# Performance work log

Measured on AMD Instinct MI355X. Metric: run time of the kernel, lower is better.

The kernel has to match this reference:

```python
import jax, jax.numpy as jnp
import numpy as np

B, S, H, D = 1, 2048, 24, 128   # batch, img seq, heads, head_dim
RD = 64                          # rotary_emb_dim (partial RoPE)
IPS, IPD = 512, 1152             # ip tokens, ip feature dim
HID = H * D                      # 3072
EPS = 1e-6


def _heads(x):
    # (B, S, H*D) -> (B, H, S, D)
    b, s, _ = x.shape
    return x.reshape(b, s, H, D).transpose(0, 2, 1, 3)


def _rmsnorm(x, scale):
    # RMSNorm with p<0 path: rms = ||x||_2 / sqrt(D); y = scale * x / (rms + eps)
    rms = jnp.linalg.norm(x, axis=-1, keepdims=True) * (D ** -0.5)
    return scale * (x / (rms + EPS))


def _rope(x, sin, cos):
    # rotate-half RoPE on first RD channels, pass-through on the rest
    xr, xp = x[..., :RD], x[..., RD:]
    x1, x2 = jnp.split(xr, 2, axis=-1)
    rot = jnp.concatenate([-x2, x1], axis=-1)
    return jnp.concatenate([xr * cos + rot * sin, xp], axis=-1)


def setup_inputs() -> dict:
    key = jax.random.key(0)
    ks = jax.random.split(key, 16)
    std = 0.02
    inp = {
        "hidden_states": jax.random.normal(ks[0], (B, S, HID), jnp.float32),
        "ip_hidden_states": jax.random.normal(ks[1], (B, IPS, IPD), jnp.float32),
        "sin": jax.random.normal(ks[2], (S, RD), jnp.float32),
        "cos": jax.random.normal(ks[3], (S, RD), jnp.float32),
        "Wq": jax.random.normal(ks[4], (HID, HID), jnp.float32) * std,
        "bq": jnp.zeros((HID,), jnp.float32),
        "Wk": jax.random.normal(ks[5], (HID, HID), jnp.float32) * std,
        "bk": jnp.zeros((HID,), jnp.float32),
        "Wv": jax.random.normal(ks[6], (HID, HID), jnp.float32) * std,
        "bv": jnp.zeros((HID,), jnp.float32),
        "Wo": jax.random.normal(ks[7], (HID, HID), jnp.float32) * std,
        "bo": jnp.zeros((HID,), jnp.float32),
        "Wk_ip": jax.random.normal(ks[8], (HID, IPD), jnp.float32) * std,
        "bk_ip": jnp.zeros((HID,), jnp.float32),
        "Wv_ip": jax.random.normal(ks[9], (HID, IPD), jnp.float32) * std,
        "bv_ip": jnp.zeros((HID,), jnp.float32),
        "q_scale": jnp.ones((D,), jnp.float32),
        "k_scale": jnp.ones((D,), jnp.float32),
    }
    return inp


def reference(hidden_states, ip_hidden_states, sin, cos,
              Wq, bq, Wk, bk, Wv, bv, Wo, bo,
              Wk_ip, bk_ip, Wv_ip, bv_ip, q_scale, k_scale):
    scale = 1.0  # default `scale` kwarg
    # projections (self-attention: encoder_hidden_states = hidden_states)
    q = _heads(hidden_states @ Wq.T + bq)        # (B,H,S,D)
    k = _heads(hidden_states @ Wk.T + bk)
    v = _heads(hidden_states @ Wv.T + bv)
    k_ip = _heads(ip_hidden_states @ Wk_ip.T + bk_ip)   # (B,H,IPS,D)
    v_ip = _heads(ip_hidden_states @ Wv_ip.T + bv_ip)

    # IP branch uses RMS-normed, head_dim^-0.5-scaled, UNROTATED q and k_ip
    # (key_ip is rotated in the source but the rotated value is never used)
    q_norm = _rmsnorm(q, q_scale) * (D ** -0.5)
    k_ip_norm = _rmsnorm(k_ip, k_scale) * (D ** -0.5)

    # main branch: RoPE'd q/k, raw dot product (alpha=1.0, no 1/sqrt(d))
    q_rot = _rope(q, sin, cos)
    k_rot = _rope(k, sin, cos)

    scores = jnp.einsum('bhsd,bhtd->bhst', q_rot, k_rot)
    probs = jax.nn.softmax(scores, axis=-1)
    scores_ip = scale * jnp.einsum('bhsd,bhtd->bhst', q_norm, k_ip_norm)
    probs_ip = jax.nn.softmax(scores_ip, axis=-1)

    out = jnp.einsum('bhst,bhtd->bhsd', probs, v) \
        + jnp.einsum('bhst,bhtd->bhsd', probs_ip, v_ip)
    out = out.transpose(0, 2, 1, 3).reshape(B, S, HID)  # batch_to_head_dim
    out = out @ Wo.T + bo                                # to_out[0]; dropout = id
    return out
```

## Files before the change

### kernel.cpp

```cpp
#include <hip/hip_runtime.h>
#include <stdint.h>

#define S_LEN 2048
#define NH    24
#define HD    128
#define HID   3072
#define IPS   512
#define IPD   1152

using f16   = __fp16;
using f16x4 = __fp16 __attribute__((ext_vector_type(4)));
using f16x8 = __fp16 __attribute__((ext_vector_type(8)));
using f32x4 = float  __attribute__((ext_vector_type(4)));
using f32x16 = float __attribute__((ext_vector_type(16)));

__device__ __forceinline__ void glds16(const f16* g, f16* l) {
  __builtin_amdgcn_global_load_lds((const __attribute__((address_space(1))) void*)g,
                                   (__attribute__((address_space(3))) void*)l,
                                   16, 0, 0);
}

struct CastArgs { const float* src[8]; f16* dst[8]; long n4[8]; };

__global__ void k_cvt_all(CastArgs a, long total4) {
  long i = blockIdx.x * 256L + threadIdx.x;
  if (i >= total4) return;
  long r = i; int s = 0;
  while (r >= a.n4[s]) { r -= a.n4[s]; s++; }
  float4 v = ((const float4*)a.src[s])[r];
  f16x4 o;
  o.x = (f16)v.x; o.y = (f16)v.y; o.z = (f16)v.z; o.w = (f16)v.w;
  ((f16x4*)a.dst[s])[r] = o;
}

struct ProjArgs {
  const f16 *A0, *A1;
  const f16 *Wq, *Wk, *Wv, *Wkip, *Wvip;
  const float *bq, *bk, *bv, *bkip, *bvip;
  f16 *q, *k, *v, *kip, *vip;
};

__global__ __launch_bounds__(256) void k_gemm_proj(ProjArgs pa) {
  const int z = blockIdx.z;
  const f16* A; const f16* B; const float* bias; f16* C; int K;
  if (z == 0)      { A = pa.A0; B = pa.Wq;   bias = pa.bq;   C = pa.q;   K = 3072; }
  else if (z == 1) { A = pa.A0; B = pa.Wk;   bias = pa.bk;   C = pa.k;   K = 3072; }
  else if (z == 2) { A = pa.A0; B = pa.Wv;   bias = pa.bv;   C = pa.v;   K = 3072; }
  else if (z == 3) { if (blockIdx.y >= 4) return;
                     A = pa.A1; B = pa.Wkip; bias = pa.bkip; C = pa.kip; K = 1152; }
  else             { if (blockIdx.y >= 4) return;
                     A = pa.A1; B = pa.Wvip; bias = pa.bvip; C = pa.vip; K = 1152; }

  __shared__ f16 As[128 * 64];
  __shared__ f16 Bs[128 * 64];

  const int tid = threadIdx.x;
  const int w   = tid >> 6, l = tid & 63;
  const int l31 = l & 31, hi = l >> 5;
  const int bm = blockIdx.y * 128, bn = blockIdx.x * 128;
  const int wm = (w >> 1) * 64,    wn = (w & 1) * 64;

  f32x16 acc[2][2] = {};

  const int r0   = w * 32;
  const int srow = l >> 3;
  const int gch  = (l & 7) ^ (srow & 7);
  const f16* Ag = A + (long)(bm + r0 + srow) * K + gch * 8;
  const f16* Bg = B + (long)(bn + r0 + srow) * K + gch * 8;
  f16* lA = &As[r0 * 64];
  f16* lB = &Bs[r0 * 64];
  const long rs8 = 8L * K;
  const int swz = l & 7;

  for (int k0 = 0; k0 < K; k0 += 64) {
#pragma unroll
    for (int g = 0; g < 4; g++) {
      glds16(Ag + g * rs8 + k0, lA + g * 512);
      glds16(Bg + g * rs8 + k0, lB + g * 512);
    }
    __syncthreads();

#pragma unroll
    for (int ks = 0; ks < 4; ks++) {
      const int pos = ((ks * 2 + hi) ^ swz) * 8;
      f16x8 af[2], bf[2];
#pragma unroll
      for (int mi = 0; mi < 2; mi++)
        af[mi] = *(const f16x8*)&As[(wm + mi * 32 + l31) * 64 + pos];
#pragma unroll
      for (int nj = 0; nj < 2; nj++)
        bf[nj] = *(const f16x8*)&Bs[(wn + nj * 32 + l31) * 64 + pos];
#pragma unroll
      for (int mi = 0; mi < 2; mi++)
#pragma unroll
        for (int nj = 0; nj < 2; nj++)
          acc[mi][nj] = __builtin_amdgcn_mfma_f32_32x32x16_f16(af[mi], bf[nj], acc[mi][nj], 0, 0, 0);
    }
    __syncthreads();
  }

#pragma unroll
  for (int mi = 0; mi < 2; mi++)
#pragma unroll
    for (int nj = 0; nj < 2; nj++) {
      const int col = bn + wn + nj * 32 + l31;
      const float bvv = bias[col];
      const int rowb = bm + wm + mi * 32 + 4 * hi;
#pragma unroll
      for (int reg = 0; reg < 16; reg++) {
        const int row = rowb + (reg & 3) + 8 * (reg >> 2);
        C[(long)row * HID + col] = (f16)(acc[mi][nj][reg] + bvv);
      }
    }
}

__global__ __launch_bounds__(256) void k_gemm_nt(
    const f16* __restrict__ A, const f16* __restrict__ B,
    const float* __restrict__ bias, float* __restrict__ Cv,
    int M, int N, int K)
{
  __shared__ f16 As[128 * 64];
  __shared__ f16 Bs[128 * 64];

  const int tid = threadIdx.x;
  const int w   = tid >> 6, l = tid & 63;
  const int l31 = l & 31, hi = l >> 5;
  const int bm = blockIdx.y * 128, bn = blockIdx.x * 128;
  const int wm = (w >> 1) * 64,    wn = (w & 1) * 64;

  f32x16 acc[2][2] = {};

  const int r0   = w * 32;
  const int srow = l >> 3;
  const int gch  = (l & 7) ^ (srow & 7);
  const f16* Ag = A + (long)(bm + r0 + srow) * K + gch * 8;
  const f16* Bg = B + (long)(bn + r0 + srow) * K + gch * 8;
  f16* lA = &As[r0 * 64];
  f16* lB = &Bs[r0 * 64];
  const long rs8 = 8L * K;
  const int swz = l & 7;

  for (int k0 = 0; k0 < K; k0 += 64) {
#pragma unroll
    for (int g = 0; g < 4; g++) {
      glds16(Ag + g * rs8 + k0, lA + g * 512);
      glds16(Bg + g * rs8 + k0, lB + g * 512);
    }
    __syncthreads();

#pragma unroll
    for (int ks = 0; ks < 4; ks++) {
      const int pos = ((ks * 2 + hi) ^ swz) * 8;
      f16x8 af[2], bf[2];
#pragma unroll
      for (int mi = 0; mi < 2; mi++)
        af[mi] = *(const f16x8*)&As[(wm + mi * 32 + l31) * 64 + pos];
#pragma unroll
      for (int nj = 0; nj < 2; nj++)
        bf[nj] = *(const f16x8*)&Bs[(wn + nj * 32 + l31) * 64 + pos];
#pragma unroll
      for (int mi = 0; mi < 2; mi++)
#pragma unroll
        for (int nj = 0; nj < 2; nj++)
          acc[mi][nj] = __builtin_amdgcn_mfma_f32_32x32x16_f16(af[mi], bf[nj], acc[mi][nj], 0, 0, 0);
    }
    __syncthreads();
  }

#pragma unroll
  for (int mi = 0; mi < 2; mi++)
#pragma unroll
    for (int nj = 0; nj < 2; nj++) {
      const int col = bn + wn + nj * 32 + l31;
      const float bvv = bias[col];
      const int rowb = bm + wm + mi * 32 + 4 * hi;
#pragma unroll
      for (int reg = 0; reg < 16; reg++) {
        const int row = rowb + (reg & 3) + 8 * (reg >> 2);
        Cv[(long)row * N + col] = acc[mi][nj][reg] + bvv;
      }
    }
}

__global__ void k_qprep(const f16* __restrict__ x, const float* __restrict__ snp,
                        const float* __restrict__ csp, const float* __restrict__ scale,
                        f16* __restrict__ qrot, f16* __restrict__ qnorm, int rows) {
  int gw = (blockIdx.x * 256 + threadIdx.x) >> 6;
  int l  = threadIdx.x & 63;
  if (gw >= rows) return;
  long base = (long)gw * HD;
  int s = gw / NH;
  int d = 2 * l;
  float a = (float)x[base + d];
  float b = (float)x[base + d + 1];

  float ss = a * a + b * b;
#pragma unroll
  for (int off = 32; off >= 1; off >>= 1) ss += __shfl_xor(ss, off, 64);
  float rms = sqrtf(ss * (1.0f / HD));
  float inv = 0.08838834764831845f / (rms + 1e-6f);
  qnorm[base + d]     = (f16)(a * scale[d] * inv);
  qnorm[base + d + 1] = (f16)(b * scale[d + 1] * inv);

  float pa = __shfl_xor(a, 16, 64);
  float pb = __shfl_xor(b, 16, 64);
  float ra, rb;
  if (d < 64) {
    float sgn = (d < 32) ? -1.0f : 1.0f;
    ra = a * csp[s * 64 + d]     + sgn * pa * snp[s * 64 + d];
    rb = b * csp[s * 64 + d + 1] + sgn * pb * snp[s * 64 + d + 1];
  } else {
    ra = a; rb = b;
  }
  qrot[base + d]     = (f16)ra;
  qrot[base + d + 1] = (f16)rb;
}

__global__ void k_krope_pack(const f16* __restrict__ src, const float* __restrict__ snp,
                             const float* __restrict__ csp, f16* __restrict__ dst,
                             int T, int nchunk) {
  int i = blockIdx.x * 256 + threadIdx.x;
  if (i >= nchunk) return;
  int d8 = i % 384;
  int t  = i / 384;
  int h  = d8 >> 4;
  int d  = (d8 & 15) * 8;
  f16x8 x = *(const f16x8*)(src + (long)i * 8);
  f16x8 o;
  if (d < 64) {
    f16x8 p = (d < 32) ? *(const f16x8*)(src + (long)i * 8 + 32)
                       : *(const f16x8*)(src + (long)i * 8 - 32);
    float sgn = (d < 32) ? -1.0f : 1.0f;
#pragma unroll
    for (int j = 0; j < 8; j++) {
      float cs = csp[t * 64 + d + j], sn = snp[t * 64 + d + j];
      o[j] = (f16)((float)x[j] * cs + sgn * (float)p[j] * sn);
    }
  } else {
    o = x;
  }
  long off = ((((long)h * (T >> 4) + (t >> 4)) * 4 + (d >> 5)) * 64 + ((d >> 3) & 3) * 16 + (t & 15)) * 8;
  *(f16x8*)(dst + off) = o;
}

__global__ void k_rms_pack(const f16* __restrict__ x, const float* __restrict__ scale,
                           f16* __restrict__ dst, int T, int rows) {
  int gw  = (blockIdx.x * 256 + threadIdx.x) >> 6;
  int l   = threadIdx.x & 63;
  int sub = l >> 4, l16 = l & 15;
  int row = gw * 4 + sub;
  if (row >= rows) return;
  int t = row / NH, h = row - t * NH;
  int d = l16 * 8;
  f16x8 v = *(const f16x8*)(x + (long)row * HD + d);
  float ss = 0.f;
#pragma unroll
  for (int j = 0; j < 8; j++) { float f = (float)v[j]; ss += f * f; }
  ss += __shfl_xor(ss, 1, 64);
  ss += __shfl_xor(ss, 2, 64);
  ss += __shfl_xor(ss, 4, 64);
  ss += __shfl_xor(ss, 8, 64);
  float rms = sqrtf(ss * (1.0f / HD));
  float inv = 0.08838834764831845f / (rms + 1e-6f);
  f16x8 o;
#pragma unroll
  for (int j = 0; j < 8; j++) o[j] = (f16)((float)v[j] * scale[d + j] * inv);
  long off = ((((long)h * (T >> 4) + (t >> 4)) * 4 + (d >> 5)) * 64 + ((d >> 3) & 3) * 16 + (t & 15)) * 8;
  *(f16x8*)(dst + off) = o;
}

__global__ __launch_bounds__(256) void k_vpack(const f16* __restrict__ v, f16* __restrict__ dst, int T) {
  __shared__ f16 Ts[128 * 72];
  int h = blockIdx.y, tb = blockIdx.x, t0 = tb * 64;
  int tid = threadIdx.x;
  int r = tid >> 2, c4 = tid & 3;
#pragma unroll
  for (int cc = 0; cc < 4; cc++) {
    int ch = c4 * 4 + cc;
    f16x8 x = *(const f16x8*)(v + (long)(t0 + r) * HID + h * HD + ch * 8);
#pragma unroll
    for (int j = 0; j < 8; j++)
      Ts[(ch * 8 + j) * 72 + r] = x[j];
  }
  __syncthreads();
  int l16 = tid & 15, jd = (tid >> 4) & 7, ks = tid >> 7;
#pragma unroll
  for (int quad = 0; quad < 4; quad++) {
    f16x8 x = *(const f16x8*)&Ts[(jd * 16 + l16) * 72 + ks * 32 + quad * 8];
    long off = ((((long)h * (T >> 6) + tb) * 2 + ks) * 8 + jd) * 512 + (quad * 16 + l16) * 8;
    *(f16x8*)(dst + off) = x;
  }
}

__global__ __launch_bounds__(256, 3) void k_flash2(
    const f16* __restrict__ Q, const f16* __restrict__ Kp, const f16* __restrict__ Vp,
    f16* __restrict__ Opart, long part_stride, float2* __restrict__ ml, int p0,
    int T, int Tc)
{
  __shared__ f16 Ps[4][32 * 72];

  const int h    = blockIdx.y;
  const int sp   = blockIdx.z;
  const int tid  = threadIdx.x, w = tid >> 6, l = tid & 63;
  const int quad = l >> 4, l16 = l & 15;
  const int qr   = blockIdx.x * 128 + w * 32;
  const int Tt16 = T >> 4, Tt64 = T >> 6;

  f16x8 qf[2][4];
#pragma unroll
  for (int mt = 0; mt < 2; mt++)
#pragma unroll
    for (int kq = 0; kq < 4; kq++)
      qf[mt][kq] = *(const f16x8*)(Q + (long)(qr + mt * 16 + l16) * HID + h * HD + kq * 32 + quad * 8);

  f32x4 o[2][8] = {};
  float m_run[8], l_run[8];
#pragma unroll
  for (int i = 0; i < 8; i++) { m_run[i] = -1e30f; l_run[i] = 0.f; }

  f16* myP = &Ps[w][0];
  const int t_begin = sp * Tc, t_end = t_begin + Tc;

  for (int t0 = t_begin; t0 < t_end; t0 += 64) {
    f32x4 s[2][4] = {};
#pragma unroll
    for (int kq = 0; kq < 4; kq++) {
      f16x8 kf[4];
#pragma unroll
      for (int jn = 0; jn < 4; jn++)
        kf[jn] = *(const f16x8*)(Kp + (((long)(h * Tt16 + (t0 >> 4) + jn) * 4 + kq) * 64 + l) * 8);
#pragma unroll
      for (int mt = 0; mt < 2; mt++)
#pragma unroll
        for (int jn = 0; jn < 4; jn++)
          s[mt][jn] = __builtin_amdgcn_mfma_f32_16x16x32_f16(qf[mt][kq], kf[jn], s[mt][jn], 0, 0, 0);
    }

#pragma unroll
    for (int mt = 0; mt < 2; mt++) {
#pragma unroll
      for (int r = 0; r < 4; r++) {
        float mx = fmaxf(fmaxf(s[mt][0][r], s[mt][1][r]), fmaxf(s[mt][2][r], s[mt][3][r]));
        mx = fmaxf(mx, __shfl_xor(mx, 1, 64));
        mx = fmaxf(mx, __shfl_xor(mx, 2, 64));
        mx = fmaxf(mx, __shfl_xor(mx, 4, 64));
        mx = fmaxf(mx, __shfl_xor(mx, 8, 64));
        const int ri = mt * 4 + r;
        float mn = fmaxf(m_run[ri], mx);
        float al = __expf(m_run[ri] - mn);
        m_run[ri] = mn;
        float p0v = __expf(s[mt][0][r] - mn);
        float p1v = __expf(s[mt][1][r] - mn);
        float p2v = __expf(s[mt][2][r] - mn);
        float p3v = __expf(s[mt][3][r] - mn);
        s[mt][0][r] = p0v; s[mt][1][r] = p1v; s[mt][2][r] = p2v; s[mt][3][r] = p3v;
        l_run[ri] = l_run[ri] * al + (p0v + p1v + p2v + p3v);
#pragma unroll
        for (int jd = 0; jd < 8; jd++) o[mt][jd][r] *= al;
      }
    }

#pragma unroll
    for (int mt = 0; mt < 2; mt++)
#pragma unroll
      for (int jn = 0; jn < 4; jn++)
#pragma unroll
        for (int r = 0; r < 4; r++)
          myP[(mt * 16 + quad * 4 + r) * 72 + jn * 16 + l16] = (f16)s[mt][jn][r];

#pragma unroll
    for (int ks = 0; ks < 2; ks++) {
      f16x8 pf[2];
#pragma unroll
      for (int mt = 0; mt < 2; mt++)
        pf[mt] = *(const f16x8*)&myP[(mt * 16 + l16) * 72 + ks * 32 + quad * 8];
      f16x8 vf[8];
#pragma unroll
      for (int jd = 0; jd < 8; jd++)
        vf[jd] = *(const f16x8*)(Vp + ((((long)(h * Tt64 + (t0 >> 6)) * 2 + ks) * 8 + jd) * 64 + l) * 8);
#pragma unroll
      for (int jd = 0; jd < 8; jd++)
#pragma unroll
        for (int mt = 0; mt < 2; mt++)
          o[mt][jd] = __builtin_amdgcn_mfma_f32_16x16x32_f16(pf[mt], vf[jd], o[mt][jd], 0, 0, 0);
    }
  }

#pragma unroll
  for (int i = 0; i < 8; i++) {
    float v = l_run[i];
    v += __shfl_xor(v, 1, 64);
    v += __shfl_xor(v, 2, 64);
    v += __shfl_xor(v, 4, 64);
    v += __shfl_xor(v, 8, 64);
    l_run[i] = v;
  }

  f16* Od = Opart + (long)sp * part_stride;
#pragma unroll
  for (int mt = 0; mt < 2; mt++)
#pragma unroll
    for (int jd = 0; jd < 8; jd++)
#pragma unroll
      for (int r = 0; r < 4; r++) {
        int row = qr + mt * 16 + quad * 4 + r;
        int col = h * HD + jd * 16 + l16;
        Od[(long)row * HID + col] = (f16)o[mt][jd][r];
      }
  if (l16 == 0) {
#pragma unroll
    for (int mt = 0; mt < 2; mt++)
#pragma unroll
      for (int r = 0; r < 4; r++) {
        int row = qr + mt * 16 + quad * 4 + r;
        float2 v; v.x = m_run[mt * 4 + r]; v.y = l_run[mt * 4 + r];
        ml[((long)(p0 + sp) * NH + h) * S_LEN + row] = v;
      }
  }
}

__global__ void k_combine(const f16* __restrict__ O0, const f16* __restrict__ O1,
                          const f16* __restrict__ O2, const f16* __restrict__ O3,
                          const f16* __restrict__ O4, const f16* __restrict__ O5,
                          const float2* __restrict__ ml, f16* __restrict__ out, int nchunk) {
  int i = blockIdx.x * 256 + threadIdx.x;
  if (i >= nchunk) return;
  int s = i / 384, d8 = i - s * 384, h = d8 >> 4;
  long base = (long)h * S_LEN + s;
  float2 a0 = ml[0 * NH * S_LEN + base];
  float2 a1 = ml[1L * NH * S_LEN + base];
  float2 a2 = ml[2L * NH * S_LEN + base];
  float2 a3 = ml[3L * NH * S_LEN + base];
  float2 a4 = ml[4L * NH * S_LEN + base];
  float2 a5 = ml[5L * NH * S_LEN + base];
  float M1 = fmaxf(fmaxf(a0.x, a1.x), fmaxf(a2.x, a3.x));
  float e0 = __expf(a0.x - M1), e1 = __expf(a1.x - M1), e2 = __expf(a2.x - M1), e3 = __expf(a3.x - M1);
  float L1 = a0.y * e0 + a1.y * e1 + a2.y * e2 + a3.y * e3;
  float w0 = e0 / L1, w1 = e1 / L1, w2 = e2 / L1, w3 = e3 / L1;
  float M2 = fmaxf(a4.x, a5.x);
  float e4 = __expf(a4.x - M2), e5 = __expf(a5.x - M2);
  float L2 = a4.y * e4 + a5.y * e5;
  float w4 = e4 / L2, w5 = e5 / L2;
  f16x8 v0 = ((const f16x8*)O0)[i];
  f16x8 v1 = ((const f16x8*)O1)[i];
  f16x8 v2 = ((const f16x8*)O2)[i];
  f16x8 v3 = ((const f16x8*)O3)[i];
  f16x8 v4 = ((const f16x8*)O4)[i];
  f16x8 v5 = ((const f16x8*)O5)[i];
  f16x8 r;
#pragma unroll
  for (int j = 0; j < 8; j++) {
    float acc = w0 * (float)v0[j] + w1 * (float)v1[j] + w2 * (float)v2[j] + w3 * (float)v3[j]
              + w4 * (float)v4[j] + w5 * (float)v5[j];
    r[j] = (f16)acc;
  }
  ((f16x8*)out)[i] = r;
}

extern "C" void kernel_launch(void* const* d_in, const int* in_sizes, int n_in,
                              void* d_out, int out_size, void* d_ws, size_t ws_size,
                              hipStream_t stream) {
  const float* hs   = (const float*)d_in[0];
  const float* ip   = (const float*)d_in[1];
  const float* snp  = (const float*)d_in[2];
  const float* csp  = (const float*)d_in[3];
  const float* Wq   = (const float*)d_in[4];
  const float* bq   = (const float*)d_in[5];
  const float* Wk   = (const float*)d_in[6];
  const float* bk   = (const float*)d_in[7];
  const float* Wv   = (const float*)d_in[8];
  const float* bv   = (const float*)d_in[9];
  const float* Wo   = (const float*)d_in[10];
  const float* bo   = (const float*)d_in[11];
  const float* Wkip = (const float*)d_in[12];
  const float* bkip = (const float*)d_in[13];
  const float* Wvip = (const float*)d_in[14];
  const float* bvip = (const float*)d_in[15];
  const float* qs   = (const float*)d_in[16];
  const float* ks   = (const float*)d_in[17];
  float* out = (float*)d_out;

  const long n1   = 6291456;
  const long nW   = 9437184;
  const long nip  = 589824;
  const long nWip = 3538944;

  const long o_hs   = 0;
  const long o_Wq   = 6291456;
  const long o_Wk   = 15728640;
  const long o_Wv   = 25165824;
  const long o_Wo   = 34603008;
  const long o_ip   = 44040192;
  const long o_Wkip = 44630016;
  const long o_Wvip = 48168960;
  const long o_q    = 51707904;
  const long o_k    = 57999360;
  const long o_v    = 64290816;
  const long o_kip  = 70582272;
  const long o_vip  = 72155136;
  const long o_qrot = 73728000;
  const long o_qnorm= 80019456;
  const long o_Vpip = 87883776;
  const long o_ml   = 89456640;
  const long o_Kps  = o_hs;
  const long o_Op0  = o_Wq;
  const long o_Op4  = o_Wkip;
  const long o_Op5  = o_q;
  const long o_Vps  = o_k;
  const long o_Kpip = o_kip;
  const long o_attn = o_v;

  f16* WS = (f16*)d_ws;
  auto P = [&](long off) { return WS + off; };
  float2* mlp = (float2*)(WS + o_ml);

  CastArgs ca;
  ca.src[0] = hs;   ca.dst[0] = P(o_hs);   ca.n4[0] = n1 / 4;
  ca.src[1] = ip;   ca.dst[1] = P(o_ip);   ca.n4[1] = nip / 4;
  ca.src[2] = Wq;   ca.dst[2] = P(o_Wq);   ca.n4[2] = nW / 4;
  ca.src[3] = Wk;   ca.dst[3] = P(o_Wk);   ca.n4[3] = nW / 4;
  ca.src[4] = Wv;   ca.dst[4] = P(o_Wv);   ca.n4[4] = nW / 4;
  ca.src[5] = Wo;   ca.dst[5] = P(o_Wo);   ca.n4[5] = nW / 4;
  ca.src[6] = Wkip; ca.dst[6] = P(o_Wkip); ca.n4[6] = nWip / 4;
  ca.src[7] = Wvip; ca.dst[7] = P(o_Wvip); ca.n4[7] = nWip / 4;
  const long total4 = (n1 + nip + 4 * nW + 2 * nWip) / 4;
  k_cvt_all<<<dim3((total4 + 255) / 256), 256, 0, stream>>>(ca, total4);

  ProjArgs pa;
  pa.A0 = P(o_hs); pa.A1 = P(o_ip);
  pa.Wq = P(o_Wq); pa.Wk = P(o_Wk); pa.Wv = P(o_Wv);
  pa.Wkip = P(o_Wkip); pa.Wvip = P(o_Wvip);
  pa.bq = bq; pa.bk = bk; pa.bv = bv; pa.bkip = bkip; pa.bvip = bvip;
  pa.q = P(o_q); pa.k = P(o_k); pa.v = P(o_v);
  pa.kip = P(o_kip); pa.vip = P(o_vip);
  k_gemm_proj<<<dim3(24, 16, 5), 256, 0, stream>>>(pa);

  k_qprep<<<dim3(49152 / 4), 256, 0, stream>>>(P(o_q), snp, csp, qs, P(o_qrot), P(o_qnorm), 49152);
  k_krope_pack<<<dim3(786432 / 256), 256, 0, stream>>>(P(o_k), snp, csp, P(o_Kps), 2048, 786432);
  k_rms_pack<<<dim3(12288 / 16), 256, 0, stream>>>(P(o_kip), ks, P(o_Kpip), 512, 12288);
  k_vpack<<<dim3(32, 24), 256, 0, stream>>>(P(o_v),   P(o_Vps),  2048);
  k_vpack<<<dim3(8, 24),  256, 0, stream>>>(P(o_vip), P(o_Vpip), 512);

  k_flash2<<<dim3(16, 24, 4), 256, 0, stream>>>(P(o_qrot), P(o_Kps), P(o_Vps),
      P(o_Op0), n1, mlp, 0, 2048, 512);
  k_flash2<<<dim3(16, 24, 2), 256, 0, stream>>>(P(o_qnorm), P(o_Kpip), P(o_Vpip),
      P(o_Op4), o_Op5 - o_Op4, mlp, 4, 512, 256);

  k_combine<<<dim3(786432 / 256), 256, 0, stream>>>(
      P(o_Op0), P(o_Op0 + n1), P(o_Op0 + 2 * n1), P(o_Op0 + 3 * n1),
      P(o_Op4), P(o_Op5), mlp, P(o_attn), 786432);

  k_gemm_nt<<<dim3(24, 16, 1), 256, 0, stream>>>(P(o_attn),
      P(o_Wo), bo, out, 2048, 3072, 3072);
}
```

Measured before the change: 668.4 us.

## Fuse fp32-to-fp16 weight conversion into GEMM B-tile loads; use DPP reductions

The separate cast kernel stops converting the weight matrices to fp16. The projection and output GEMMs now read fp32 weights directly, convert them in registers and store them to LDS, while the activations still use async global-to-LDS loads. This removes a large weight write and re-read pass through memory. In exchange, each GEMM tile reads twice the bytes for B, and the B-tile loads become synchronous register loads with conversion inside the main loop. The flash-attention row max and sum reductions also switch from shuffles to DPP moves.

```diff
diff --git a/kernel.cpp b/kernel.cpp
--- a/kernel.cpp
+++ b/kernel.cpp
@@ -20,29 +20,44 @@
                                    16, 0, 0);
 }
 
-struct CastArgs { const float* src[8]; f16* dst[8]; long n4[8]; };
-
-__global__ void k_cvt_all(CastArgs a, long total4) {
+__device__ __forceinline__ float red16_max(float x) {
+  x = fmaxf(x, __int_as_float(__builtin_amdgcn_mov_dpp(__float_as_int(x), 0xB1, 0xf, 0xf, true)));
+  x = fmaxf(x, __int_as_float(__builtin_amdgcn_mov_dpp(__float_as_int(x), 0x4E, 0xf, 0xf, true)));
+  x = fmaxf(x, __int_as_float(__builtin_amdgcn_mov_dpp(__float_as_int(x), 0x141, 0xf, 0xf, true)));
+  x = fmaxf(x, __int_as_float(__builtin_amdgcn_mov_dpp(__float_as_int(x), 0x140, 0xf, 0xf, true)));
+  return x;
+}
+__device__ __forceinline__ float red16_sum(float x) {
+  x += __int_as_float(__builtin_amdgcn_mov_dpp(__float_as_int(x), 0xB1, 0xf, 0xf, true));
+  x += __int_as_float(__builtin_amdgcn_mov_dpp(__float_as_int(x), 0x4E, 0xf, 0xf, true));
+  x += __int_as_float(__builtin_amdgcn_mov_dpp(__float_as_int(x), 0x141, 0xf, 0xf, true));
+  x += __int_as_float(__builtin_amdgcn_mov_dpp(__float_as_int(x), 0x140, 0xf, 0xf, true));
+  return x;
+}
+
+__global__ void k_cvt2(const float* __restrict__ a, f16* __restrict__ da, long n4a,
+                       const float* __restrict__ b, f16* __restrict__ db, long total4) {
   long i = blockIdx.x * 256L + threadIdx.x;
   if (i >= total4) return;
-  long r = i; int s = 0;
-  while (r >= a.n4[s]) { r -= a.n4[s]; s++; }
-  float4 v = ((const float4*)a.src[s])[r];
+  const float* s; f16* d; long r;
+  if (i < n4a) { s = a; d = da; r = i; }
+  else         { s = b; d = db; r = i - n4a; }
+  float4 v = ((const float4*)s)[r];
   f16x4 o;
   o.x = (f16)v.x; o.y = (f16)v.y; o.z = (f16)v.z; o.w = (f16)v.w;
-  ((f16x4*)a.dst[s])[r] = o;
+  ((f16x4*)d)[r] = o;
 }
 
 struct ProjArgs {
   const f16 *A0, *A1;
-  const f16 *Wq, *Wk, *Wv, *Wkip, *Wvip;
+  const float *Wq, *Wk, *Wv, *Wkip, *Wvip;
   const float *bq, *bk, *bv, *bkip, *bvip;
   f16 *q, *k, *v, *kip, *vip;
 };
 
 __global__ __launch_bounds__(256) void k_gemm_proj(ProjArgs pa) {
   const int z = blockIdx.z;
-  const f16* A; const f16* B; const float* bias; f16* C; int K;
+  const f16* A; const float* B; const float* bias; f16* C; int K;
   if (z == 0)      { A = pa.A0; B = pa.Wq;   bias = pa.bq;   C = pa.q;   K = 3072; }
   else if (z == 1) { A = pa.A0; B = pa.Wk;   bias = pa.bk;   C = pa.k;   K = 3072; }
   else if (z == 2) { A = pa.A0; B = pa.Wv;   bias = pa.bv;   C = pa.v;   K = 3072; }
@@ -65,8 +80,8 @@
   const int r0   = w * 32;
   const int srow = l >> 3;
   const int gch  = (l & 7) ^ (srow & 7);
-  const f16* Ag = A + (long)(bm + r0 + srow) * K + gch * 8;
-  const f16* Bg = B + (long)(bn + r0 + srow) * K + gch * 8;
+  const f16*   Ag = A + (long)(bm + r0 + srow) * K + gch * 8;
+  const float* Bg = B + (long)(bn + r0 + srow) * K + gch * 8;
   f16* lA = &As[r0 * 64];
   f16* lB = &Bs[r0 * 64];
   const long rs8 = 8L * K;
@@ -74,9 +89,17 @@
 
   for (int k0 = 0; k0 < K; k0 += 64) {
 #pragma unroll
+    for (int g = 0; g < 4; g++)
+      glds16(Ag + g * rs8 + k0, lA + g * 512);
+#pragma unroll
     for (int g = 0; g < 4; g++) {
-      glds16(Ag + g * rs8 + k0, lA + g * 512);
-      glds16(Bg + g * rs8 + k0, lB + g * 512);
+      const float* src = Bg + g * rs8 + k0;
+      float4 u0 = *(const float4*)src;
+      float4 u1 = *(const float4*)(src + 4);
+      f16x8 hh;
+      hh[0] = (f16)u0.x; hh[1] = (f16)u0.y; hh[2] = (f16)u0.z; hh[3] = (f16)u0.w;
+      hh[4] = (f16)u1.x; hh[5] = (f16)u1.y; hh[6] = (f16)u1.z; hh[7] = (f16)u1.w;
+      *(f16x8*)(lB + g * 512 + l * 8) = hh;
     }
     __syncthreads();
 
@@ -115,7 +138,7 @@
 }
 
 __global__ __launch_bounds__(256) void k_gemm_nt(
-    const f16* __restrict__ A, const f16* __restrict__ B,
+    const f16* __restrict__ A, const float* __restrict__ B,
     const float* __restrict__ bias, float* __restrict__ Cv,
     int M, int N, int K)
 {
@@ -133,8 +156,8 @@
   const int r0   = w * 32;
   const int srow = l >> 3;
   const int gch  = (l & 7) ^ (srow & 7);
-  const f16* Ag = A + (long)(bm + r0 + srow) * K + gch * 8;
-  const f16* Bg = B + (long)(bn + r0 + srow) * K + gch * 8;
+  const f16*   Ag = A + (long)(bm + r0 + srow) * K + gch * 8;
+  const float* Bg = B + (long)(bn + r0 + srow) * K + gch * 8;
   f16* lA = &As[r0 * 64];
   f16* lB = &Bs[r0 * 64];
   const long rs8 = 8L * K;
@@ -142,9 +165,17 @@
 
   for (int k0 = 0; k0 < K; k0 += 64) {
 #pragma unroll
+    for (int g = 0; g < 4; g++)
+      glds16(Ag + g * rs8 + k0, lA + g * 512);
+#pragma unroll
     for (int g = 0; g < 4; g++) {
-      glds16(Ag + g * rs8 + k0, lA + g * 512);
-      glds16(Bg + g * rs8 + k0, lB + g * 512);
+      const float* src = Bg + g * rs8 + k0;
+      float4 u0 = *(const float4*)src;
+      float4 u1 = *(const float4*)(src + 4);
+      f16x8 hh;
+      hh[0] = (f16)u0.x; hh[1] = (f16)u0.y; hh[2] = (f16)u0.z; hh[3] = (f16)u0.w;
+      hh[4] = (f16)u1.x; hh[5] = (f16)u1.y; hh[6] = (f16)u1.z; hh[7] = (f16)u1.w;
+      *(f16x8*)(lB + g * 512 + l * 8) = hh;
     }
     __syncthreads();
 
@@ -341,10 +372,7 @@
 #pragma unroll
       for (int r = 0; r < 4; r++) {
         float mx = fmaxf(fmaxf(s[mt][0][r], s[mt][1][r]), fmaxf(s[mt][2][r], s[mt][3][r]));
-        mx = fmaxf(mx, __shfl_xor(mx, 1, 64));
-        mx = fmaxf(mx, __shfl_xor(mx, 2, 64));
-        mx = fmaxf(mx, __shfl_xor(mx, 4, 64));
-        mx = fmaxf(mx, __shfl_xor(mx, 8, 64));
+        mx = red16_max(mx);
         const int ri = mt * 4 + r;
         float mn = fmaxf(m_run[ri], mx);
         float al = __expf(m_run[ri] - mn);
@@ -387,14 +415,8 @@
   }
 
 #pragma unroll
-  for (int i = 0; i < 8; i++) {
-    float v = l_run[i];
-    v += __shfl_xor(v, 1, 64);
-    v += __shfl_xor(v, 2, 64);
-    v += __shfl_xor(v, 4, 64);
-    v += __shfl_xor(v, 8, 64);
-    l_run[i] = v;
-  }
+  for (int i = 0; i < 8; i++)
+    l_run[i] = red16_sum(l_run[i]);
 
   f16* Od = Opart + (long)sp * part_stride;
 #pragma unroll
@@ -481,18 +503,12 @@
   float* out = (float*)d_out;
 
   const long n1   = 6291456;
-  const long nW   = 9437184;
   const long nip  = 589824;
-  const long nWip = 3538944;
 
   const long o_hs   = 0;
   const long o_Wq   = 6291456;
-  const long o_Wk   = 15728640;
-  const long o_Wv   = 25165824;
-  const long o_Wo   = 34603008;
+  const long o_Wkip = 44630016;
   const long o_ip   = 44040192;
-  const long o_Wkip = 44630016;
-  const long o_Wvip = 48168960;
   const long o_q    = 51707904;
   const long o_k    = 57999360;
   const long o_v    = 64290816;
@@ -514,22 +530,14 @@
   auto P = [&](long off) { return WS + off; };
   float2* mlp = (float2*)(WS + o_ml);
 
-  CastArgs ca;
-  ca.src[0] = hs;   ca.dst[0] = P(o_hs);   ca.n4[0] = n1 / 4;
-  ca.src[1] = ip;   ca.dst[1] = P(o_ip);   ca.n4[1] = nip / 4;
-  ca.src[2] = Wq;   ca.dst[2] = P(o_Wq);   ca.n4[2] = nW / 4;
-  ca.src[3] = Wk;   ca.dst[3] = P(o_Wk);   ca.n4[3] = nW / 4;
-  ca.src[4] = Wv;   ca.dst[4] = P(o_Wv);   ca.n4[4] = nW / 4;
-  ca.src[5] = Wo;   ca.dst[5] = P(o_Wo);   ca.n4[5] = nW / 4;
-  ca.src[6] = Wkip; ca.dst[6] = P(o_Wkip); ca.n4[6] = nWip / 4;
-  ca.src[7] = Wvip; ca.dst[7] = P(o_Wvip); ca.n4[7] = nWip / 4;
-  const long total4 = (n1 + nip + 4 * nW + 2 * nWip) / 4;
-  k_cvt_all<<<dim3((total4 + 255) / 256), 256, 0, stream>>>(ca, total4);
+  const long total4 = (n1 + nip) / 4;
+  k_cvt2<<<dim3((total4 + 255) / 256), 256, 0, stream>>>(
+      hs, P(o_hs), n1 / 4, ip, P(o_ip), total4);
 
   ProjArgs pa;
   pa.A0 = P(o_hs); pa.A1 = P(o_ip);
-  pa.Wq = P(o_Wq); pa.Wk = P(o_Wk); pa.Wv = P(o_Wv);
-  pa.Wkip = P(o_Wkip); pa.Wvip = P(o_Wvip);
+  pa.Wq = Wq; pa.Wk = Wk; pa.Wv = Wv;
+  pa.Wkip = Wkip; pa.Wvip = Wvip;
   pa.bq = bq; pa.bk = bk; pa.bv = bv; pa.bkip = bkip; pa.bvip = bvip;
   pa.q = P(o_q); pa.k = P(o_k); pa.v = P(o_v);
   pa.kip = P(o_kip); pa.vip = P(o_vip);
@@ -551,5 +559,5 @@
       P(o_Op4), P(o_Op5), mlp, P(o_attn), 786432);
 
   k_gemm_nt<<<dim3(24, 16, 1), 256, 0, stream>>>(P(o_attn),
-      P(o_Wo), bo, out, 2048, 3072, 3072);
-}
+      Wo, bo, out, 2048, 3072, 3072);
+}
```

Result: faster. 636.3 us (-4.8%).
